# Optimization experiments

Measured on AMD Instinct MI355X. Metric: run time of the kernel, lower is better.

Reference implementation:

```python
import jax, jax.numpy as jnp
import numpy as np

B, H, S, DK = 2, 16, 2048, 64


def setup_inputs() -> dict:
    key = jax.random.key(0)
    kq, kk, kv = jax.random.split(key, 3)
    Q = jax.random.normal(kq, (B, H, S, DK), dtype=jnp.float32)
    K = jax.random.normal(kk, (B, H, S, DK), dtype=jnp.float32)
    V = jax.random.normal(kv, (B, H, S, DK), dtype=jnp.float32)
    # causal mask: True = attend, broadcast to [B, H, S, S]
    causal = jnp.tril(jnp.ones((S, S), dtype=jnp.bool_))
    mask = jnp.broadcast_to(causal, (B, H, S, S))
    return {"d_model": 1024, "num_heads": 16, "Q": Q, "K": K, "V": V, "mask": mask}


def reference(d_model, num_heads, Q, K, V, mask):
    dk = Q.shape[-1]
    # scores: [B, H, Sq, Sk] -- naive full materialization, matching the torch code
    scores = jnp.einsum("bhqd,bhkd->bhqk", Q, K) / jnp.sqrt(jnp.asarray(dk, Q.dtype))
    scores = jnp.where(mask, scores, -jnp.inf)
    attn = jax.nn.softmax(scores, axis=-1)
    return jnp.einsum("bhqk,bhkd->bhqd", attn, V)
```

## Files before the change

### kernel.cpp

```cpp
#include <hip/hip_runtime.h>
#include <hip/hip_bf16.h>


using bf16x8 = __attribute__((ext_vector_type(8))) short;
using f32x4  = __attribute__((ext_vector_type(4))) float;

#define SEQ 2048
#define DKK 64

__device__ __forceinline__ short f2bf(float f) {
    union { float f; unsigned u; } v; v.f = f;
    unsigned r = v.u + 0x7fffu + ((v.u >> 16) & 1u);
    return (short)(r >> 16);
}

__global__ __launch_bounds__(256, 4)
void fa_fwd(const float* __restrict__ Qg, const float* __restrict__ Kg,
            const float* __restrict__ Vg, float* __restrict__ Og) {
    __shared__ short Kt[32 * 72];
    __shared__ short Vt[64 * 40];
    __shared__ short Ps[4 * 16 * 40];

    const int qblk = (int)gridDim.x - 1 - (int)blockIdx.x;
    const int bh   = blockIdx.y;
    const int qb0  = qblk * 64;
    const int tid  = threadIdx.x;
    const int lane = tid & 63;
    const int w    = tid >> 6;
    const int m16  = lane & 15;
    const int quad = lane >> 4;

    const size_t hoff = (size_t)bh * SEQ * DKK;
    const float* Qh = Qg + hoff;
    const float* Kh = Kg + hoff;
    const float* Vh = Vg + hoff;
    float*       Oh = Og + hoff;

    const int qb   = qb0 + 16 * w;
    const int qrow = qb + m16;

    bf16x8 qf[2];
    {
        const float* qp = Qh + (size_t)qrow * DKK + quad * 8;
        #pragma unroll
        for (int h = 0; h < 2; ++h) {
            f32x4 a = *(const f32x4*)(qp + 32 * h);
            f32x4 b = *(const f32x4*)(qp + 32 * h + 4);
            bf16x8 f;
            f[0] = f2bf(a[0]); f[1] = f2bf(a[1]); f[2] = f2bf(a[2]); f[3] = f2bf(a[3]);
            f[4] = f2bf(b[0]); f[5] = f2bf(b[1]); f[6] = f2bf(b[2]); f[7] = f2bf(b[3]);
            qf[h] = f;
        }
    }

    float mrun = -1e30f, lrun = 0.f;
    f32x4 acc[4];
    {
        f32x4 z = {0.f, 0.f, 0.f, 0.f};
        #pragma unroll
        for (int c = 0; c < 4; ++c) acc[c] = z;
    }

    const int T = 2 * qblk + 2;
    for (int t = 0; t < T; ++t) {
        const int kb = t * 32;
        __syncthreads();
        {
            const int n = tid >> 3, c = tid & 7;
            const float* sp = Kh + (size_t)(kb + n) * DKK + c * 8;
            f32x4 a = *(const f32x4*)sp;
            f32x4 b = *(const f32x4*)(sp + 4);
            bf16x8 f;
            f[0] = f2bf(a[0]); f[1] = f2bf(a[1]); f[2] = f2bf(a[2]); f[3] = f2bf(a[3]);
            f[4] = f2bf(b[0]); f[5] = f2bf(b[1]); f[6] = f2bf(b[2]); f[7] = f2bf(b[3]);
            *(bf16x8*)&Kt[n * 72 + c * 8] = f;
        }
        {
            const int n0 = (tid & 15) * 2, d0 = (tid >> 4) * 4;
            const float* v0 = Vh + (size_t)(kb + n0) * DKK + d0;
            f32x4 a = *(const f32x4*)v0;
            f32x4 b = *(const f32x4*)(v0 + DKK);
            #pragma unroll
            for (int i = 0; i < 4; ++i) {
                unsigned pk = ((unsigned)(unsigned short)f2bf(a[i])) |
                              ((unsigned)(unsigned short)f2bf(b[i]) << 16);
                *(unsigned*)&Vt[(d0 + i) * 40 + n0] = pk;
            }
        }
        __syncthreads();

        if (kb > qb + 15) continue;

        f32x4 st0 = {0.f, 0.f, 0.f, 0.f}, st1 = {0.f, 0.f, 0.f, 0.f};
        {
            const bf16x8 k00 = *(const bf16x8*)&Kt[m16 * 72 + quad * 8];
            const bf16x8 k01 = *(const bf16x8*)&Kt[m16 * 72 + 32 + quad * 8];
            const bf16x8 k10 = *(const bf16x8*)&Kt[(16 + m16) * 72 + quad * 8];
            const bf16x8 k11 = *(const bf16x8*)&Kt[(16 + m16) * 72 + 32 + quad * 8];
            st0 = __builtin_amdgcn_mfma_f32_16x16x32_bf16(k00, qf[0], st0, 0, 0, 0);
            st0 = __builtin_amdgcn_mfma_f32_16x16x32_bf16(k01, qf[1], st0, 0, 0, 0);
            st1 = __builtin_amdgcn_mfma_f32_16x16x32_bf16(k10, qf[0], st1, 0, 0, 0);
            st1 = __builtin_amdgcn_mfma_f32_16x16x32_bf16(k11, qf[1], st1, 0, 0, 0);
        }

        const float cs = 0.18033688011112042f;
        float x[8];
        #pragma unroll
        for (int r = 0; r < 4; ++r) { x[r] = st0[r] * cs; x[4 + r] = st1[r] * cs; }
        if (kb + 31 > qb) {
            #pragma unroll
            for (int i = 0; i < 8; ++i) {
                const int n = kb + (i >> 2) * 16 + quad * 4 + (i & 3);
                if (n > qrow) x[i] = -1e30f;
            }
        }

        float mx = x[0];
        #pragma unroll
        for (int i = 1; i < 8; ++i) mx = fmaxf(mx, x[i]);
        mx = fmaxf(mx, __shfl_xor(mx, 16));
        mx = fmaxf(mx, __shfl_xor(mx, 32));
        const float mnew  = fmaxf(mrun, mx);
        const float alpha = exp2f(mrun - mnew);
        float p[8], psum = 0.f;
        #pragma unroll
        for (int i = 0; i < 8; ++i) { p[i] = exp2f(x[i] - mnew); psum += p[i]; }
        psum += __shfl_xor(psum, 16);
        psum += __shfl_xor(psum, 32);
        lrun = lrun * alpha + psum;
        mrun = mnew;
        #pragma unroll
        for (int c = 0; c < 4; ++c) {
            #pragma unroll
            for (int r = 0; r < 4; ++r) acc[c][r] *= alpha;
        }

        short* ps = &Ps[w * 640];
        #pragma unroll
        for (int i = 0; i < 8; ++i)
            ps[m16 * 40 + (i >> 2) * 16 + quad * 4 + (i & 3)] = f2bf(p[i]);
        __threadfence_block();
        const bf16x8 pf = *(const bf16x8*)&Ps[w * 640 + m16 * 40 + quad * 8];

        #pragma unroll
        for (int c = 0; c < 4; ++c) {
            const bf16x8 vf = *(const bf16x8*)&Vt[(c * 16 + m16) * 40 + quad * 8];
            acc[c] = __builtin_amdgcn_mfma_f32_16x16x32_bf16(vf, pf, acc[c], 0, 0, 0);
        }
    }

    const float inv = 1.0f / lrun;
    float* op = Oh + (size_t)qrow * DKK;
    #pragma unroll
    for (int c = 0; c < 4; ++c) {
        #pragma unroll
        for (int r = 0; r < 4; ++r)
            op[c * 16 + quad * 4 + r] = acc[c][r] * inv;
    }
}

extern "C" void kernel_launch(void* const* d_in, const int* in_sizes, int n_in,
                              void* d_out, int out_size, void* d_ws, size_t ws_size,
                              hipStream_t stream) {
    const float* Q = (const float*)d_in[2];
    const float* K = (const float*)d_in[3];
    const float* V = (const float*)d_in[4];
    float* O = (float*)d_out;
    (void)in_sizes; (void)n_in; (void)out_size; (void)d_ws; (void)ws_size;
    dim3 grid(SEQ / 64, 32 );
    fa_fwd<<<grid, 256, 0, stream>>>(Q, K, V, O);
}
```

Before: 717.1 us.

## Double-buffer 64-wide K/V tiles with register prefetch and fold scale into Q

New measurement: 700.6 us. -2.3%, faster.

```diff
diff --git a/kernel.cpp b/kernel.cpp
--- a/kernel.cpp
+++ b/kernel.cpp
@@ -3,10 +3,12 @@
 
 
 using bf16x8 = __attribute__((ext_vector_type(8))) short;
+using bf16x4 = __attribute__((ext_vector_type(4))) short;
 using f32x4  = __attribute__((ext_vector_type(4))) float;
 
-#define SEQ 2048
-#define DKK 64
+#define SEQ  2048
+#define DKK  64
+#define KSTR 72
 
 __device__ __forceinline__ short f2bf(float f) {
     union { float f; unsigned u; } v; v.f = f;
@@ -14,16 +16,15 @@
     return (short)(r >> 16);
 }
 
-__global__ __launch_bounds__(256, 4)
+__global__ __launch_bounds__(256, 3)
 void fa_fwd(const float* __restrict__ Qg, const float* __restrict__ Kg,
             const float* __restrict__ Vg, float* __restrict__ Og) {
-    __shared__ short Kt[32 * 72];
-    __shared__ short Vt[64 * 40];
-    __shared__ short Ps[4 * 16 * 40];
+    __shared__ short Kt[2][64 * KSTR];
+    __shared__ short Vt[2][64 * KSTR];
+    __shared__ short Ps[4][16 * KSTR];
 
     const int qblk = (int)gridDim.x - 1 - (int)blockIdx.x;
     const int bh   = blockIdx.y;
-    const int qb0  = qblk * 64;
     const int tid  = threadIdx.x;
     const int lane = tid & 63;
     const int w    = tid >> 6;
@@ -36,9 +37,13 @@
     const float* Vh = Vg + hoff;
     float*       Oh = Og + hoff;
 
-    const int qb   = qb0 + 16 * w;
+    const int qb   = qblk * 64 + 16 * w;
     const int qrow = qb + m16;
 
+    const int kn = tid >> 2, kc = tid & 3;
+    const int vn = (tid & 31) * 2, vd = (tid >> 5) * 8;
+
+    const float cs = 0.18033688011112042f;
     bf16x8 qf[2];
     {
         const float* qp = Qh + (size_t)qrow * DKK + quad * 8;
@@ -47,8 +52,10 @@
             f32x4 a = *(const f32x4*)(qp + 32 * h);
             f32x4 b = *(const f32x4*)(qp + 32 * h + 4);
             bf16x8 f;
-            f[0] = f2bf(a[0]); f[1] = f2bf(a[1]); f[2] = f2bf(a[2]); f[3] = f2bf(a[3]);
-            f[4] = f2bf(b[0]); f[5] = f2bf(b[1]); f[6] = f2bf(b[2]); f[7] = f2bf(b[3]);
+            f[0] = f2bf(a[0] * cs); f[1] = f2bf(a[1] * cs);
+            f[2] = f2bf(a[2] * cs); f[3] = f2bf(a[3] * cs);
+            f[4] = f2bf(b[0] * cs); f[5] = f2bf(b[1] * cs);
+            f[6] = f2bf(b[2] * cs); f[7] = f2bf(b[3] * cs);
             qf[h] = f;
         }
     }
@@ -61,70 +68,81 @@
         for (int c = 0; c < 4; ++c) acc[c] = z;
     }
 
-    const int T = 2 * qblk + 2;
+    f32x4 kr[4], vr[4];
+    auto load_tile = [&](int kb) {
+        const float* kp = Kh + (size_t)(kb + kn) * DKK + kc * 16;
+        #pragma unroll
+        for (int i = 0; i < 4; ++i) kr[i] = *(const f32x4*)(kp + 4 * i);
+        const float* vp = Vh + (size_t)(kb + vn) * DKK + vd;
+        vr[0] = *(const f32x4*)vp;        vr[1] = *(const f32x4*)(vp + 4);
+        vr[2] = *(const f32x4*)(vp + DKK); vr[3] = *(const f32x4*)(vp + DKK + 4);
+    };
+    auto store_tile = [&](int buf) {
+        bf16x8 f0, f1;
+        #pragma unroll
+        for (int i = 0; i < 4; ++i) { f0[i] = f2bf(kr[0][i]); f0[4+i] = f2bf(kr[1][i]); }
+        #pragma unroll
+        for (int i = 0; i < 4; ++i) { f1[i] = f2bf(kr[2][i]); f1[4+i] = f2bf(kr[3][i]); }
+        *(bf16x8*)&Kt[buf][kn * KSTR + kc * 16]     = f0;
+        *(bf16x8*)&Kt[buf][kn * KSTR + kc * 16 + 8] = f1;
+        #pragma unroll
+        for (int i = 0; i < 8; ++i) {
+            float a = (i < 4) ? vr[0][i] : vr[1][i - 4];
+            float b = (i < 4) ? vr[2][i] : vr[3][i - 4];
+            unsigned pk = ((unsigned)(unsigned short)f2bf(a)) |
+                          ((unsigned)(unsigned short)f2bf(b) << 16);
+            *(unsigned*)&Vt[buf][(vd + i) * KSTR + vn] = pk;
+        }
+    };
+
+    const int T = qblk + 1;
+    load_tile(0);
+    store_tile(0);
+    __syncthreads();
+
     for (int t = 0; t < T; ++t) {
-        const int kb = t * 32;
-        __syncthreads();
-        {
-            const int n = tid >> 3, c = tid & 7;
-            const float* sp = Kh + (size_t)(kb + n) * DKK + c * 8;
-            f32x4 a = *(const f32x4*)sp;
-            f32x4 b = *(const f32x4*)(sp + 4);
-            bf16x8 f;
-            f[0] = f2bf(a[0]); f[1] = f2bf(a[1]); f[2] = f2bf(a[2]); f[3] = f2bf(a[3]);
-            f[4] = f2bf(b[0]); f[5] = f2bf(b[1]); f[6] = f2bf(b[2]); f[7] = f2bf(b[3]);
-            *(bf16x8*)&Kt[n * 72 + c * 8] = f;
-        }
-        {
-            const int n0 = (tid & 15) * 2, d0 = (tid >> 4) * 4;
-            const float* v0 = Vh + (size_t)(kb + n0) * DKK + d0;
-            f32x4 a = *(const f32x4*)v0;
-            f32x4 b = *(const f32x4*)(v0 + DKK);
+        const int cur = t & 1;
+        const int kb  = t * 64;
+        if (t + 1 < T) load_tile((t + 1) * 64);
+
+        f32x4 st[4];
+        #pragma unroll
+        for (int c = 0; c < 4; ++c) {
+            f32x4 z = {0.f, 0.f, 0.f, 0.f};
+            const bf16x8 k0 = *(const bf16x8*)&Kt[cur][(16 * c + m16) * KSTR + quad * 8];
+            const bf16x8 k1 = *(const bf16x8*)&Kt[cur][(16 * c + m16) * KSTR + 32 + quad * 8];
+            z = __builtin_amdgcn_mfma_f32_16x16x32_bf16(k0, qf[0], z, 0, 0, 0);
+            z = __builtin_amdgcn_mfma_f32_16x16x32_bf16(k1, qf[1], z, 0, 0, 0);
+            st[c] = z;
+        }
+
+        float x[16];
+        #pragma unroll
+        for (int c = 0; c < 4; ++c) {
             #pragma unroll
-            for (int i = 0; i < 4; ++i) {
-                unsigned pk = ((unsigned)(unsigned short)f2bf(a[i])) |
-                              ((unsigned)(unsigned short)f2bf(b[i]) << 16);
-                *(unsigned*)&Vt[(d0 + i) * 40 + n0] = pk;
+            for (int r = 0; r < 4; ++r) x[4 * c + r] = st[c][r];
+        }
+        if (t == T - 1) {
+            #pragma unroll
+            for (int c = 0; c < 4; ++c) {
+                #pragma unroll
+                for (int r = 0; r < 4; ++r) {
+                    const int n = kb + 16 * c + quad * 4 + r;
+                    if (n > qrow) x[4 * c + r] = -1e30f;
+                }
             }
         }
-        __syncthreads();
-
-        if (kb > qb + 15) continue;
-
-        f32x4 st0 = {0.f, 0.f, 0.f, 0.f}, st1 = {0.f, 0.f, 0.f, 0.f};
-        {
-            const bf16x8 k00 = *(const bf16x8*)&Kt[m16 * 72 + quad * 8];
-            const bf16x8 k01 = *(const bf16x8*)&Kt[m16 * 72 + 32 + quad * 8];
-            const bf16x8 k10 = *(const bf16x8*)&Kt[(16 + m16) * 72 + quad * 8];
-            const bf16x8 k11 = *(const bf16x8*)&Kt[(16 + m16) * 72 + 32 + quad * 8];
-            st0 = __builtin_amdgcn_mfma_f32_16x16x32_bf16(k00, qf[0], st0, 0, 0, 0);
-            st0 = __builtin_amdgcn_mfma_f32_16x16x32_bf16(k01, qf[1], st0, 0, 0, 0);
-            st1 = __builtin_amdgcn_mfma_f32_16x16x32_bf16(k10, qf[0], st1, 0, 0, 0);
-            st1 = __builtin_amdgcn_mfma_f32_16x16x32_bf16(k11, qf[1], st1, 0, 0, 0);
-        }
-
-        const float cs = 0.18033688011112042f;
-        float x[8];
-        #pragma unroll
-        for (int r = 0; r < 4; ++r) { x[r] = st0[r] * cs; x[4 + r] = st1[r] * cs; }
-        if (kb + 31 > qb) {
-            #pragma unroll
-            for (int i = 0; i < 8; ++i) {
-                const int n = kb + (i >> 2) * 16 + quad * 4 + (i & 3);
-                if (n > qrow) x[i] = -1e30f;
-            }
-        }
 
         float mx = x[0];
         #pragma unroll
-        for (int i = 1; i < 8; ++i) mx = fmaxf(mx, x[i]);
+        for (int i = 1; i < 16; ++i) mx = fmaxf(mx, x[i]);
         mx = fmaxf(mx, __shfl_xor(mx, 16));
         mx = fmaxf(mx, __shfl_xor(mx, 32));
         const float mnew  = fmaxf(mrun, mx);
         const float alpha = exp2f(mrun - mnew);
-        float p[8], psum = 0.f;
-        #pragma unroll
-        for (int i = 0; i < 8; ++i) { p[i] = exp2f(x[i] - mnew); psum += p[i]; }
+        float p[16], psum = 0.f;
+        #pragma unroll
+        for (int i = 0; i < 16; ++i) { p[i] = exp2f(x[i] - mnew); psum += p[i]; }
         psum += __shfl_xor(psum, 16);
         psum += __shfl_xor(psum, 32);
         lrun = lrun * alpha + psum;
@@ -135,18 +153,29 @@
             for (int r = 0; r < 4; ++r) acc[c][r] *= alpha;
         }
 
-        short* ps = &Ps[w * 640];
-        #pragma unroll
-        for (int i = 0; i < 8; ++i)
-            ps[m16 * 40 + (i >> 2) * 16 + quad * 4 + (i & 3)] = f2bf(p[i]);
+        short* ps = &Ps[w][0];
+        #pragma unroll
+        for (int c = 0; c < 4; ++c) {
+            bf16x4 pk;
+            pk[0] = f2bf(p[4*c]); pk[1] = f2bf(p[4*c+1]);
+            pk[2] = f2bf(p[4*c+2]); pk[3] = f2bf(p[4*c+3]);
+            *(bf16x4*)&ps[m16 * KSTR + 16 * c + quad * 4] = pk;
+        }
         __threadfence_block();
-        const bf16x8 pf = *(const bf16x8*)&Ps[w * 640 + m16 * 40 + quad * 8];
-
-        #pragma unroll
-        for (int c = 0; c < 4; ++c) {
-            const bf16x8 vf = *(const bf16x8*)&Vt[(c * 16 + m16) * 40 + quad * 8];
-            acc[c] = __builtin_amdgcn_mfma_f32_16x16x32_bf16(vf, pf, acc[c], 0, 0, 0);
-        }
+        bf16x8 pf[2];
+        pf[0] = *(const bf16x8*)&ps[m16 * KSTR + quad * 8];
+        pf[1] = *(const bf16x8*)&ps[m16 * KSTR + 32 + quad * 8];
+
+        #pragma unroll
+        for (int c = 0; c < 4; ++c) {
+            const bf16x8 v0 = *(const bf16x8*)&Vt[cur][(16 * c + m16) * KSTR + quad * 8];
+            const bf16x8 v1 = *(const bf16x8*)&Vt[cur][(16 * c + m16) * KSTR + 32 + quad * 8];
+            acc[c] = __builtin_amdgcn_mfma_f32_16x16x32_bf16(v0, pf[0], acc[c], 0, 0, 0);
+            acc[c] = __builtin_amdgcn_mfma_f32_16x16x32_bf16(v1, pf[1], acc[c], 0, 0, 0);
+        }
+
+        if (t + 1 < T) store_tile(cur ^ 1);
+        __syncthreads();
     }
 
     const float inv = 1.0f / lrun;
```
